# Performance work log

Hardware: AMD Instinct MI355X
Metric: run time of the kernel (lower is better)

The kernel has to match this reference:

```python
import jax, jax.numpy as jnp
import numpy as np

SIGMA = 30.0   # noise scale (init kwarg)
T = 0.5        # diffusion time used to set heat-kernel width
B, NC = 524288, 3


def _sigma_func(sigma, t):
    # std dev of Euclidean heat kernel at time t
    return np.sqrt((sigma ** (2.0 * t) - 1.0) / (2.0 * np.log(sigma)))


def setup_inputs() -> dict:
    key = jax.random.key(0)
    k1, k2, k3, k4, k5 = jax.random.split(key, 5)
    sigma_t = np.float32(_sigma_func(SIGMA, T))

    # eigenvalue angles of the su(N) algebra element (heat-kernel sample proxy),
    # projected traceless so exp(i*diag(xs)) has unit determinant
    xs = jax.random.normal(k1, (B, NC), dtype=jnp.float32) * sigma_t
    xs = xs - jnp.mean(xs, axis=-1, keepdims=True)

    # Haar-random unitary V via QR of a complex Gaussian matrix
    V, _ = jnp.linalg.qr(jax.random.normal(k2, (B, NC, NC), dtype=jnp.float32)
                         + 1j * jax.random.normal(k3, (B, NC, NC), dtype=jnp.float32))
    # random unitary starting configuration U_0
    U0, _ = jnp.linalg.qr(jax.random.normal(k4, (B, NC, NC), dtype=jnp.float32)
                          + 1j * jax.random.normal(k5, (B, NC, NC), dtype=jnp.float32))

    return {
        "U0_re": jnp.asarray(U0.real, jnp.float32),
        "U0_im": jnp.asarray(U0.imag, jnp.float32),
        "xs": xs,
        "V_re": jnp.asarray(V.real, jnp.float32),
        "V_im": jnp.asarray(V.imag, jnp.float32),
    }


def reference(U0_re, U0_im, xs, V_re, V_im):
    # U_t = exp(1j * V diag(xs) V^H) @ U_0
    # Since V is unitary, expm(i V diag(xs) V^H) = V diag(exp(i xs)) V^H exactly
    # (closed-form Lie-algebra exponential; same math as matrix_exp on the
    #  conjugated skew-Hermitian generator).
    V = V_re + 1j * V_im                       # [B, Nc, Nc]
    U0 = U0_re + 1j * U0_im                    # [B, Nc, Nc]
    phases = jnp.exp(1j * xs)                  # [B, Nc]
    Vh = jnp.conj(jnp.swapaxes(V, -1, -2))     # V^H
    E = (V * phases[:, None, :]) @ Vh          # expm(1j * A), unitary [B, Nc, Nc]
    Ut = E @ U0                                # diffused configuration
    # return real/imag stacked so the output is a real float array
    return jnp.stack([Ut.real, Ut.imag], axis=-1)  # [B, Nc, Nc, 2]
```

## Files before the change

### kernel.cpp

```cpp
#include <hip/hip_runtime.h>


#define BPB 256

__global__ __launch_bounds__(256, 4)
void sun_diffuse_kernel(const float* __restrict__ U0_re, const float* __restrict__ U0_im,
                        const float* __restrict__ xs,
                        const float* __restrict__ V_re, const float* __restrict__ V_im,
                        float* __restrict__ out, int nb)
{
    __shared__ float smem[4][2496];

    const int tid  = threadIdx.x;
    const int w    = tid >> 6;
    const int lane = tid & 63;
    const int b0   = blockIdx.x * BPB;
    const int nblk = min(BPB, nb - b0);
    const bool full = (nblk == BPB);

    float* S     = smem[w];
    float* sVre  = S;
    float* sVim  = S + 576;
    float* sU0re = S + 1152;
    float* sU0im = S + 1728;
    float* sxs   = S + 2304;

    const int wb0 = b0 + w * 64;
    const int nw  = min(max(nblk - w * 64, 0), 64);

    if (full) {
        const float4* g0 = reinterpret_cast<const float4*>(V_re  + (size_t)wb0 * 9);
        const float4* g1 = reinterpret_cast<const float4*>(V_im  + (size_t)wb0 * 9);
        const float4* g2 = reinterpret_cast<const float4*>(U0_re + (size_t)wb0 * 9);
        const float4* g3 = reinterpret_cast<const float4*>(U0_im + (size_t)wb0 * 9);
        float4* s0 = reinterpret_cast<float4*>(sVre);
        float4* s1 = reinterpret_cast<float4*>(sVim);
        float4* s2 = reinterpret_cast<float4*>(sU0re);
        float4* s3 = reinterpret_cast<float4*>(sU0im);
#pragma unroll
        for (int r = 0; r < 3; ++r) {
            int i = lane + r * 64;
            if (i < 144) { s0[i] = g0[i]; s1[i] = g1[i]; s2[i] = g2[i]; s3[i] = g3[i]; }
        }
        if (lane < 48)
            reinterpret_cast<float4*>(sxs)[lane] =
                reinterpret_cast<const float4*>(xs + (size_t)wb0 * 3)[lane];
    } else {
        for (int i = lane; i < nw * 9; i += 64) {
            sVre[i]  = V_re [(size_t)wb0 * 9 + i];
            sVim[i]  = V_im [(size_t)wb0 * 9 + i];
            sU0re[i] = U0_re[(size_t)wb0 * 9 + i];
            sU0im[i] = U0_im[(size_t)wb0 * 9 + i];
        }
        for (int i = lane; i < nw * 3; i += 64) sxs[i] = xs[(size_t)wb0 * 3 + i];
    }

    float outr[9], outi[9];
    if (lane < nw) {
        float vr[9], vi[9], ur[9], ui[9];
#pragma unroll
        for (int m = 0; m < 9; ++m) {
            vr[m] = sVre [lane * 9 + m];
            vi[m] = sVim [lane * 9 + m];
            ur[m] = sU0re[lane * 9 + m];
            ui[m] = sU0im[lane * 9 + m];
        }
        float pr[3], pi[3];
#pragma unroll
        for (int k = 0; k < 3; ++k) {
            float s, c;
            __sincosf(sxs[lane * 3 + k], &s, &c);
            pr[k] = c; pi[k] = s;
        }
        float Er[9], Ei[9];
#pragma unroll
        for (int i = 0; i < 3; ++i) {
#pragma unroll
            for (int j = 0; j < 3; ++j) {
                float er = 0.f, ei = 0.f;
#pragma unroll
                for (int k = 0; k < 3; ++k) {
                    float wr = pr[k] * vr[i * 3 + k] - pi[k] * vi[i * 3 + k];
                    float wi = pr[k] * vi[i * 3 + k] + pi[k] * vr[i * 3 + k];
                    er += wr * vr[j * 3 + k] + wi * vi[j * 3 + k];
                    ei += wi * vr[j * 3 + k] - wr * vi[j * 3 + k];
                }
                Er[i * 3 + j] = er; Ei[i * 3 + j] = ei;
            }
        }
#pragma unroll
        for (int i = 0; i < 3; ++i) {
#pragma unroll
            for (int j = 0; j < 3; ++j) {
                float r = 0.f, im = 0.f;
#pragma unroll
                for (int k = 0; k < 3; ++k) {
                    r  += Er[i * 3 + k] * ur[k * 3 + j] - Ei[i * 3 + k] * ui[k * 3 + j];
                    im += Er[i * 3 + k] * ui[k * 3 + j] + Ei[i * 3 + k] * ur[k * 3 + j];
                }
                outr[i * 3 + j] = r; outi[i * 3 + j] = im;
            }
        }
    }

    float* sOut = S;
    if (lane < nw) {
#pragma unroll
        for (int m = 0; m < 9; ++m) {
            sOut[lane * 18 + 2 * m]     = outr[m];
            sOut[lane * 18 + 2 * m + 1] = outi[m];
        }
    }

    if (full) {
        float4* gO = reinterpret_cast<float4*>(out + (size_t)wb0 * 18);
        const float4* s = reinterpret_cast<const float4*>(sOut);
#pragma unroll
        for (int r = 0; r < 5; ++r) {
            int i = lane + r * 64;
            if (i < 288) gO[i] = s[i];
        }
    } else {
        for (int i = lane; i < nw * 18; i += 64) out[(size_t)wb0 * 18 + i] = sOut[i];
    }
}

extern "C" void kernel_launch(void* const* d_in, const int* in_sizes, int n_in,
                              void* d_out, int out_size, void* d_ws, size_t ws_size,
                              hipStream_t stream) {
    const float* U0_re = (const float*)d_in[0];
    const float* U0_im = (const float*)d_in[1];
    const float* xs    = (const float*)d_in[2];
    const float* V_re  = (const float*)d_in[3];
    const float* V_im  = (const float*)d_in[4];
    float* out = (float*)d_out;

    const int nb = in_sizes[2] / 3;
    const int grid = (nb + BPB - 1) / BPB;
    sun_diffuse_kernel<<<grid, 256, 0, stream>>>(U0_re, U0_im, xs, V_re, V_im, out, nb);
}
```

Measured before the change: 25.79 us.

## Load inputs directly from global memory and use nontemporal output stores

Drops the LDS staging of V, U0 and xs. Each lane now reads its own matrices straight from global memory with strided scalar loads, and the U0 loads are deferred until after E is computed. Output is still transposed through a smaller LDS buffer, but stored with nontemporal float4 writes, and the occupancy hint is raised to 5 blocks per SM. This saves LDS traffic and space, at the cost of uncoalesced 36-byte-stride global reads that depend on caches to merge accesses.

After: 47.95 us. 1.86x slower.

```diff
diff --git a/kernel.cpp b/kernel.cpp
--- a/kernel.cpp
+++ b/kernel.cpp
@@ -3,73 +3,35 @@
 
 #define BPB 256
 
-__global__ __launch_bounds__(256, 4)
+typedef float f32x4 __attribute__((ext_vector_type(4)));
+
+__global__ __launch_bounds__(256, 5)
 void sun_diffuse_kernel(const float* __restrict__ U0_re, const float* __restrict__ U0_im,
                         const float* __restrict__ xs,
                         const float* __restrict__ V_re, const float* __restrict__ V_im,
                         float* __restrict__ out, int nb)
 {
-    __shared__ float smem[4][2496];
+    __shared__ float sOut[4][1152];
 
     const int tid  = threadIdx.x;
     const int w    = tid >> 6;
     const int lane = tid & 63;
-    const int b0   = blockIdx.x * BPB;
-    const int nblk = min(BPB, nb - b0);
-    const bool full = (nblk == BPB);
-
-    float* S     = smem[w];
-    float* sVre  = S;
-    float* sVim  = S + 576;
-    float* sU0re = S + 1152;
-    float* sU0im = S + 1728;
-    float* sxs   = S + 2304;
-
-    const int wb0 = b0 + w * 64;
-    const int nw  = min(max(nblk - w * 64, 0), 64);
-
-    if (full) {
-        const float4* g0 = reinterpret_cast<const float4*>(V_re  + (size_t)wb0 * 9);
-        const float4* g1 = reinterpret_cast<const float4*>(V_im  + (size_t)wb0 * 9);
-        const float4* g2 = reinterpret_cast<const float4*>(U0_re + (size_t)wb0 * 9);
-        const float4* g3 = reinterpret_cast<const float4*>(U0_im + (size_t)wb0 * 9);
-        float4* s0 = reinterpret_cast<float4*>(sVre);
-        float4* s1 = reinterpret_cast<float4*>(sVim);
-        float4* s2 = reinterpret_cast<float4*>(sU0re);
-        float4* s3 = reinterpret_cast<float4*>(sU0im);
-#pragma unroll
-        for (int r = 0; r < 3; ++r) {
-            int i = lane + r * 64;
-            if (i < 144) { s0[i] = g0[i]; s1[i] = g1[i]; s2[i] = g2[i]; s3[i] = g3[i]; }
-        }
-        if (lane < 48)
-            reinterpret_cast<float4*>(sxs)[lane] =
-                reinterpret_cast<const float4*>(xs + (size_t)wb0 * 3)[lane];
-    } else {
-        for (int i = lane; i < nw * 9; i += 64) {
-            sVre[i]  = V_re [(size_t)wb0 * 9 + i];
-            sVim[i]  = V_im [(size_t)wb0 * 9 + i];
-            sU0re[i] = U0_re[(size_t)wb0 * 9 + i];
-            sU0im[i] = U0_im[(size_t)wb0 * 9 + i];
-        }
-        for (int i = lane; i < nw * 3; i += 64) sxs[i] = xs[(size_t)wb0 * 3 + i];
-    }
+    const int wb0  = blockIdx.x * BPB + w * 64;
+    const int nw   = min(max(nb - wb0, 0), 64);
 
     float outr[9], outi[9];
     if (lane < nw) {
-        float vr[9], vi[9], ur[9], ui[9];
+        const size_t mb = (size_t)(wb0 + lane) * 9;
+        const size_t xb = (size_t)(wb0 + lane) * 3;
+
+        float vr[9], vi[9];
 #pragma unroll
-        for (int m = 0; m < 9; ++m) {
-            vr[m] = sVre [lane * 9 + m];
-            vi[m] = sVim [lane * 9 + m];
-            ur[m] = sU0re[lane * 9 + m];
-            ui[m] = sU0im[lane * 9 + m];
-        }
+        for (int m = 0; m < 9; ++m) { vr[m] = V_re[mb + m]; vi[m] = V_im[mb + m]; }
         float pr[3], pi[3];
 #pragma unroll
         for (int k = 0; k < 3; ++k) {
             float s, c;
-            __sincosf(sxs[lane * 3 + k], &s, &c);
+            __sincosf(xs[xb + k], &s, &c);
             pr[k] = c; pi[k] = s;
         }
         float Er[9], Ei[9];
@@ -88,6 +50,10 @@
                 Er[i * 3 + j] = er; Ei[i * 3 + j] = ei;
             }
         }
+
+        float ur[9], ui[9];
+#pragma unroll
+        for (int m = 0; m < 9; ++m) { ur[m] = U0_re[mb + m]; ui[m] = U0_im[mb + m]; }
 #pragma unroll
         for (int i = 0; i < 3; ++i) {
 #pragma unroll
@@ -103,25 +69,25 @@
         }
     }
 
-    float* sOut = S;
+    float* S = sOut[w];
     if (lane < nw) {
 #pragma unroll
         for (int m = 0; m < 9; ++m) {
-            sOut[lane * 18 + 2 * m]     = outr[m];
-            sOut[lane * 18 + 2 * m + 1] = outi[m];
+            S[lane * 18 + 2 * m]     = outr[m];
+            S[lane * 18 + 2 * m + 1] = outi[m];
         }
     }
 
-    if (full) {
-        float4* gO = reinterpret_cast<float4*>(out + (size_t)wb0 * 18);
-        const float4* s = reinterpret_cast<const float4*>(sOut);
+    if (nw == 64) {
+        f32x4* gO = reinterpret_cast<f32x4*>(out + (size_t)wb0 * 18);
+        const f32x4* s = reinterpret_cast<const f32x4*>(S);
 #pragma unroll
         for (int r = 0; r < 5; ++r) {
             int i = lane + r * 64;
-            if (i < 288) gO[i] = s[i];
+            if (i < 288) __builtin_nontemporal_store(s[i], &gO[i]);
         }
-    } else {
-        for (int i = lane; i < nw * 18; i += 64) out[(size_t)wb0 * 18 + i] = sOut[i];
+    } else if (nw > 0) {
+        for (int i = lane; i < nw * 18; i += 64) out[(size_t)wb0 * 18 + i] = S[i];
     }
 }
 
```
